# Performance work log

Measured on AMD Instinct MI355X. Metric: run time of the kernel, lower is better.

Reference implementation:

```python
import jax, jax.numpy as jnp
import numpy as np

B, L = 64, 2048
N_RESTYPE, N_GROUP, N_ATOM = 21, 8, 14


def _compose(R1, t1, R2, t2):
    # rigid compose: (R1,t1) o (R2,t2) = (R1@R2, R1@t2 + t1)
    R = jnp.einsum('...ij,...jk->...ik', R1, R2)
    t = jnp.einsum('...ij,...j->...i', R1, t2) + t1
    return R, t


def setup_inputs() -> dict:
    key = jax.random.key(0)
    ks = jax.random.split(key, 8)
    return {
        'bb_rots': jax.random.normal(ks[0], (B, L, 3, 3), jnp.float32),
        'bb_trans': jax.random.normal(ks[1], (B, L, 3), jnp.float32),
        'angles': jax.random.normal(ks[2], (B, L, 7, 2), jnp.float32),
        'aatype': jax.random.randint(ks[3], (B, L), 0, N_RESTYPE),
        'default_frames': jax.random.normal(ks[4], (N_RESTYPE, N_GROUP, 4, 4), jnp.float32),
        'group_idx': jax.random.randint(ks[5], (N_RESTYPE, N_ATOM), 0, N_GROUP),
        'atom_mask': jax.random.uniform(ks[6], (N_RESTYPE, N_ATOM), jnp.float32),
        'lit_positions': jax.random.normal(ks[7], (N_RESTYPE, N_ATOM, 3), jnp.float32),
    }


def reference(bb_rots, bb_trans, angles, aatype, default_frames, group_idx, atom_mask, lit_positions):
    # ---- torsion_angles_to_frames ----
    d4 = default_frames[aatype]                      # [B,L,8,4,4]
    dR, dt = d4[..., :3, :3], d4[..., :3, 3]
    # prepend identity backbone torsion (sin=0, cos=1)
    bb = jnp.broadcast_to(jnp.array([0.0, 1.0], angles.dtype), (*angles.shape[:-2], 1, 2))
    ang = jnp.concatenate([bb, angles], axis=-2)     # [B,L,8,2]
    s, c = ang[..., 0], ang[..., 1]
    z, o = jnp.zeros_like(s), jnp.ones_like(s)
    # rotation about x-axis built from (sin, cos)
    rotx = jnp.stack([
        jnp.stack([o, z, z], axis=-1),
        jnp.stack([z, c, -s], axis=-1),
        jnp.stack([z, s, c], axis=-1),
    ], axis=-2)                                      # [B,L,8,3,3]
    fR = jnp.einsum('blgij,blgjk->blgik', dR, rotx)  # default_r.compose(all_rots)
    ft = dt                                          # all_rots has zero translation
    # chain chi2..chi4 onto chi1
    R5, t5 = _compose(fR[:, :, 4], ft[:, :, 4], fR[:, :, 5], ft[:, :, 5])
    R6, t6 = _compose(R5, t5, fR[:, :, 6], ft[:, :, 6])
    R7, t7 = _compose(R6, t6, fR[:, :, 7], ft[:, :, 7])
    Rbb = jnp.concatenate([fR[:, :, :5], R5[:, :, None], R6[:, :, None], R7[:, :, None]], axis=2)
    tbb = jnp.concatenate([ft[:, :, :5], t5[:, :, None], t6[:, :, None], t7[:, :, None]], axis=2)
    # compose with global backbone frame
    Rg = jnp.einsum('blij,blgjk->blgik', bb_rots, Rbb)          # [B,L,8,3,3]
    tg = jnp.einsum('blij,blgj->blgi', bb_rots, tbb) + bb_trans[:, :, None]

    # ---- frames_and_literature_positions_to_atom14_pos ----
    gidx = group_idx[aatype]                                    # [B,L,14]
    Ra = jnp.take_along_axis(Rg, gidx[:, :, :, None, None], axis=2)  # [B,L,14,3,3]
    ta = jnp.take_along_axis(tg, gidx[:, :, :, None], axis=2)        # [B,L,14,3]
    lit = lit_positions[aatype]                                 # [B,L,14,3]
    mask = atom_mask[aatype][..., None]                         # [B,L,14,1]
    pred = jnp.einsum('blaij,blaj->blai', Ra, lit) + ta
    return pred * mask
```

## Files before the change

kernel.cpp:

```cpp
#include <hip/hip_runtime.h>


constexpr int NRES_TOTAL = 64 * 2048;
constexpr int NRT = 21;
constexpr int NG  = 8;
constexpr int NA  = 14;
constexpr int BLK = 256;
constexpr int RPB = BLK / 4;

__global__ __launch_bounds__(256) void protein_mapper_kernel(
    const float* __restrict__ bb_rots,
    const float* __restrict__ bb_trans,
    const float* __restrict__ angles,
    const int*   __restrict__ aatype,
    const float* __restrict__ default_frames,
    const int*   __restrict__ group_idx,
    const float* __restrict__ atom_mask,
    const float* __restrict__ lit_positions,
    float* __restrict__ out)
{
    __shared__ float s_frames[128 * NRT];
    __shared__ int   s_gidx[NA * NRT];
    __shared__ float s_mask[NA * NRT];
    __shared__ float s_lit[NA * 3 * NRT];

    const int t   = threadIdx.x;
    const int res = blockIdx.x * RPB + (t >> 2);
    const int sub = t & 3;

    const int aa_early = aatype[res];
    float2 ang[7];
    {
        const float2* angp = reinterpret_cast<const float2*>(angles + (size_t)res * 14);
        #pragma unroll
        for (int g = 0; g < 7; ++g) ang[g] = angp[g];
    }
    const float* br = bb_rots + (size_t)res * 9;
    const float b00 = br[0], b01 = br[1], b02 = br[2];
    const float b10 = br[3], b11 = br[4], b12 = br[5];
    const float b20 = br[6], b21 = br[7], b22 = br[8];
    const float* btp = bb_trans + (size_t)res * 3;
    const float bt0 = btp[0], bt1 = btp[1], bt2 = btp[2];

    for (int n = t; n < NRT * 128; n += BLK) {
        const int aa = n / 128, j = n % 128;
        s_frames[j * NRT + aa] = default_frames[n];
    }
    for (int n = t; n < NRT * NA; n += BLK) {
        const int aa = n / NA, a = n % NA;
        s_gidx[a * NRT + aa] = group_idx[n];
        s_mask[a * NRT + aa] = atom_mask[n];
    }
    for (int n = t; n < NRT * NA * 3; n += BLK) {
        const int aa = n / (NA * 3), k = n % (NA * 3);
        s_lit[k * NRT + aa] = lit_positions[n];
    }
    __syncthreads();

    const int aa = aa_early;

    float sv[NG], cv[NG];
    sv[0] = 0.0f; cv[0] = 1.0f;
    #pragma unroll
    for (int g = 1; g < NG; ++g) { sv[g] = ang[g - 1].x; cv[g] = ang[g - 1].y; }

    float G[NG][12];
    #pragma unroll
    for (int g = 0; g < NG; ++g) {
        const float cg = cv[g], sg = sv[g];
        #pragma unroll
        for (int r = 0; r < 3; ++r) {
            const float a0 = s_frames[(g * 16 + r * 4 + 0) * NRT + aa];
            const float a1 = s_frames[(g * 16 + r * 4 + 1) * NRT + aa];
            const float a2 = s_frames[(g * 16 + r * 4 + 2) * NRT + aa];
            const float a3 = s_frames[(g * 16 + r * 4 + 3) * NRT + aa];
            G[g][r * 3 + 0] = a0;
            G[g][r * 3 + 1] = cg * a1 + sg * a2;
            G[g][r * 3 + 2] = cg * a2 - sg * a1;
            G[g][9 + r]     = a3;
        }
    }

    #pragma unroll
    for (int g = 5; g < NG; ++g) {
        float Q[12];
        #pragma unroll
        for (int r = 0; r < 3; ++r) {
            const float p0 = G[g - 1][r * 3 + 0];
            const float p1 = G[g - 1][r * 3 + 1];
            const float p2 = G[g - 1][r * 3 + 2];
            #pragma unroll
            for (int cdx = 0; cdx < 3; ++cdx)
                Q[r * 3 + cdx] = p0 * G[g][cdx] + p1 * G[g][3 + cdx] + p2 * G[g][6 + cdx];
            Q[9 + r] = p0 * G[g][9] + p1 * G[g][10] + p2 * G[g][11] + G[g - 1][9 + r];
        }
        #pragma unroll
        for (int k = 0; k < 12; ++k) G[g][k] = Q[k];
    }

    float q[12];
    #pragma unroll
    for (int j = 0; j < 4; ++j) {
        const int a = 4 * sub + j;
        if (a < NA) {
            const int   ga = s_gidx[a * NRT + aa];
            const float m_ = s_mask[a * NRT + aa];
            const float lx = s_lit[(a * 3 + 0) * NRT + aa];
            const float ly = s_lit[(a * 3 + 1) * NRT + aa];
            const float lz = s_lit[(a * 3 + 2) * NRT + aa];
            const bool b0_ = ga & 1, b1_ = ga & 2, b2_ = ga & 4;
            float S[12];
            #pragma unroll
            for (int e = 0; e < 12; ++e) {
                const float t0 = b0_ ? G[1][e] : G[0][e];
                const float t1 = b0_ ? G[3][e] : G[2][e];
                const float t2 = b0_ ? G[5][e] : G[4][e];
                const float t3 = b0_ ? G[7][e] : G[6][e];
                const float u0 = b1_ ? t1 : t0;
                const float u1 = b1_ ? t3 : t2;
                S[e] = b2_ ? u1 : u0;
            }
            const float px = S[0] * lx + S[1] * ly + S[2] * lz + S[9];
            const float py = S[3] * lx + S[4] * ly + S[5] * lz + S[10];
            const float pz = S[6] * lx + S[7] * ly + S[8] * lz + S[11];
            q[j * 3 + 0] = (b00 * px + b01 * py + b02 * pz + bt0) * m_;
            q[j * 3 + 1] = (b10 * px + b11 * py + b12 * pz + bt1) * m_;
            q[j * 3 + 2] = (b20 * px + b21 * py + b22 * pz + bt2) * m_;
        }
    }

    float2* o2 = reinterpret_cast<float2*>(out) + (size_t)res * 21 + sub * 6;
    const int nf2 = (sub == 3) ? 3 : 6;
    #pragma unroll
    for (int k = 0; k < 6; ++k) {
        if (k < nf2) {
            float2 v; v.x = q[2 * k + 0]; v.y = q[2 * k + 1];
            o2[k] = v;
        }
    }
}

extern "C" void kernel_launch(void* const* d_in, const int* in_sizes, int n_in,
                              void* d_out, int out_size, void* d_ws, size_t ws_size,
                              hipStream_t stream) {
    const float* bb_rots        = (const float*)d_in[0];
    const float* bb_trans       = (const float*)d_in[1];
    const float* angles         = (const float*)d_in[2];
    const int*   aatype         = (const int*)d_in[3];
    const float* default_frames = (const float*)d_in[4];
    const int*   group_idx      = (const int*)d_in[5];
    const float* atom_mask      = (const float*)d_in[6];
    const float* lit_positions  = (const float*)d_in[7];
    float* out = (float*)d_out;

    const int blocks = NRES_TOTAL / RPB;
    protein_mapper_kernel<<<blocks, BLK, 0, stream>>>(
        bb_rots, bb_trans, angles, aatype,
        default_frames, group_idx, atom_mask, lit_positions, out);
}
```

Measured before the change: 106.5 us.

## Split per-residue frame work across eight threads with shared-memory frame exchange

Each residue is now handled by eight threads instead of four. Each thread builds one torsion group frame, the frames are exchanged through a new shared-memory buffer, and threads 5-7 compose the chi chain from it. Atoms are then assigned two per thread and look up their frame from shared memory instead of doing register select chains. This cuts per-thread register pressure and redundant frame computation, at the cost of extra __syncthreads, extra shared memory, uneven chain work, and scalar strided output stores in place of float2 stores.

```diff
diff --git a/kernel.cpp b/kernel.cpp
--- a/kernel.cpp
+++ b/kernel.cpp
@@ -5,10 +5,11 @@
 constexpr int NRT = 21;
 constexpr int NG  = 8;
 constexpr int NA  = 14;
-constexpr int BLK = 256;
-constexpr int RPB = BLK / 4;
+constexpr int BLK = 512;
+constexpr int RPB = BLK / NG;
+constexpr int RIG_STRIDE = 100;
 
-__global__ __launch_bounds__(256) void protein_mapper_kernel(
+__global__ __launch_bounds__(512) void protein_mapper_kernel(
     const float* __restrict__ bb_rots,
     const float* __restrict__ bb_trans,
     const float* __restrict__ angles,
@@ -23,25 +24,9 @@
     __shared__ int   s_gidx[NA * NRT];
     __shared__ float s_mask[NA * NRT];
     __shared__ float s_lit[NA * 3 * NRT];
+    __shared__ float s_rig[RPB * RIG_STRIDE];
 
-    const int t   = threadIdx.x;
-    const int res = blockIdx.x * RPB + (t >> 2);
-    const int sub = t & 3;
-
-    const int aa_early = aatype[res];
-    float2 ang[7];
-    {
-        const float2* angp = reinterpret_cast<const float2*>(angles + (size_t)res * 14);
-        #pragma unroll
-        for (int g = 0; g < 7; ++g) ang[g] = angp[g];
-    }
-    const float* br = bb_rots + (size_t)res * 9;
-    const float b00 = br[0], b01 = br[1], b02 = br[2];
-    const float b10 = br[3], b11 = br[4], b12 = br[5];
-    const float b20 = br[6], b21 = br[7], b22 = br[8];
-    const float* btp = bb_trans + (size_t)res * 3;
-    const float bt0 = btp[0], bt1 = btp[1], bt2 = btp[2];
-
+    const int t = threadIdx.x;
     for (int n = t; n < NRT * 128; n += BLK) {
         const int aa = n / 128, j = n % 128;
         s_frames[j * NRT + aa] = default_frames[n];
@@ -55,87 +40,103 @@
         const int aa = n / (NA * 3), k = n % (NA * 3);
         s_lit[k * NRT + aa] = lit_positions[n];
     }
+
+    const int lres = t >> 3;
+    const int sub  = t & 7;
+    const int res  = blockIdx.x * RPB + lres;
+    const int aa   = aatype[res];
+
+    float sg_ = 0.0f, cg_ = 1.0f;
+    if (sub != 0) {
+        const float2 sc = *reinterpret_cast<const float2*>(
+            angles + (size_t)res * 14 + (size_t)(sub - 1) * 2);
+        sg_ = sc.x; cg_ = sc.y;
+    }
     __syncthreads();
 
-    const int aa = aa_early;
+    float F[12];
+    #pragma unroll
+    for (int r = 0; r < 3; ++r) {
+        const float a0 = s_frames[(sub * 16 + r * 4 + 0) * NRT + aa];
+        const float a1 = s_frames[(sub * 16 + r * 4 + 1) * NRT + aa];
+        const float a2 = s_frames[(sub * 16 + r * 4 + 2) * NRT + aa];
+        const float a3 = s_frames[(sub * 16 + r * 4 + 3) * NRT + aa];
+        F[r * 3 + 0] = a0;
+        F[r * 3 + 1] = cg_ * a1 + sg_ * a2;
+        F[r * 3 + 2] = cg_ * a2 - sg_ * a1;
+        F[9 + r]     = a3;
+    }
 
-    float sv[NG], cv[NG];
-    sv[0] = 0.0f; cv[0] = 1.0f;
-    #pragma unroll
-    for (int g = 1; g < NG; ++g) { sv[g] = ang[g - 1].x; cv[g] = ang[g - 1].y; }
+    float* rig = s_rig + lres * RIG_STRIDE;
+    {
+        float4* dst = reinterpret_cast<float4*>(rig + sub * 12);
+        float4 w0; w0.x = F[0]; w0.y = F[1];  w0.z = F[2];  w0.w = F[3];
+        float4 w1; w1.x = F[4]; w1.y = F[5];  w1.z = F[6];  w1.w = F[7];
+        float4 w2; w2.x = F[8]; w2.y = F[9];  w2.z = F[10]; w2.w = F[11];
+        dst[0] = w0; dst[1] = w1; dst[2] = w2;
+    }
+    __syncthreads();
 
-    float G[NG][12];
-    #pragma unroll
-    for (int g = 0; g < NG; ++g) {
-        const float cg = cv[g], sg = sv[g];
-        #pragma unroll
-        for (int r = 0; r < 3; ++r) {
-            const float a0 = s_frames[(g * 16 + r * 4 + 0) * NRT + aa];
-            const float a1 = s_frames[(g * 16 + r * 4 + 1) * NRT + aa];
-            const float a2 = s_frames[(g * 16 + r * 4 + 2) * NRT + aa];
-            const float a3 = s_frames[(g * 16 + r * 4 + 3) * NRT + aa];
-            G[g][r * 3 + 0] = a0;
-            G[g][r * 3 + 1] = cg * a1 + sg * a2;
-            G[g][r * 3 + 2] = cg * a2 - sg * a1;
-            G[g][9 + r]     = a3;
+    float P[12];
+    if (sub >= 5) {
+        const float4* f4 = reinterpret_cast<const float4*>(rig + 4 * 12);
+        float4 p0 = f4[0], p1 = f4[1], p2 = f4[2];
+        P[0]=p0.x; P[1]=p0.y; P[2]=p0.z; P[3]=p0.w;
+        P[4]=p1.x; P[5]=p1.y; P[6]=p1.z; P[7]=p1.w;
+        P[8]=p2.x; P[9]=p2.y; P[10]=p2.z; P[11]=p2.w;
+        for (int g = 5; g <= sub; ++g) {
+            const float4* fg = reinterpret_cast<const float4*>(rig + g * 12);
+            const float4 l0 = fg[0], l1 = fg[1], l2 = fg[2];
+            const float L[12] = {l0.x,l0.y,l0.z,l0.w,l1.x,l1.y,l1.z,l1.w,
+                                 l2.x,l2.y,l2.z,l2.w};
+            float Q[12];
+            #pragma unroll
+            for (int r = 0; r < 3; ++r) {
+                const float p0_ = P[r*3+0], p1_ = P[r*3+1], p2_ = P[r*3+2];
+                #pragma unroll
+                for (int c = 0; c < 3; ++c)
+                    Q[r*3+c] = p0_ * L[c] + p1_ * L[3+c] + p2_ * L[6+c];
+                Q[9+r] = p0_ * L[9] + p1_ * L[10] + p2_ * L[11] + P[9+r];
+            }
+            #pragma unroll
+            for (int k = 0; k < 12; ++k) P[k] = Q[k];
         }
     }
+    __syncthreads();
+    if (sub >= 5) {
+        float4* dst = reinterpret_cast<float4*>(rig + sub * 12);
+        float4 w0; w0.x = P[0]; w0.y = P[1];  w0.z = P[2];  w0.w = P[3];
+        float4 w1; w1.x = P[4]; w1.y = P[5];  w1.z = P[6];  w1.w = P[7];
+        float4 w2; w2.x = P[8]; w2.y = P[9];  w2.z = P[10]; w2.w = P[11];
+        dst[0] = w0; dst[1] = w1; dst[2] = w2;
+    }
+    __syncthreads();
+
+    const float* br = bb_rots + (size_t)res * 9;
+    const float b00 = br[0], b01 = br[1], b02 = br[2];
+    const float b10 = br[3], b11 = br[4], b12 = br[5];
+    const float b20 = br[6], b21 = br[7], b22 = br[8];
+    const float* btp = bb_trans + (size_t)res * 3;
+    const float bt0 = btp[0], bt1 = btp[1], bt2 = btp[2];
 
     #pragma unroll
-    for (int g = 5; g < NG; ++g) {
-        float Q[12];
-        #pragma unroll
-        for (int r = 0; r < 3; ++r) {
-            const float p0 = G[g - 1][r * 3 + 0];
-            const float p1 = G[g - 1][r * 3 + 1];
-            const float p2 = G[g - 1][r * 3 + 2];
-            #pragma unroll
-            for (int cdx = 0; cdx < 3; ++cdx)
-                Q[r * 3 + cdx] = p0 * G[g][cdx] + p1 * G[g][3 + cdx] + p2 * G[g][6 + cdx];
-            Q[9 + r] = p0 * G[g][9] + p1 * G[g][10] + p2 * G[g][11] + G[g - 1][9 + r];
-        }
-        #pragma unroll
-        for (int k = 0; k < 12; ++k) G[g][k] = Q[k];
-    }
-
-    float q[12];
-    #pragma unroll
-    for (int j = 0; j < 4; ++j) {
-        const int a = 4 * sub + j;
+    for (int k = 0; k < 2; ++k) {
+        const int a = sub + k * 8;
         if (a < NA) {
             const int   ga = s_gidx[a * NRT + aa];
             const float m_ = s_mask[a * NRT + aa];
             const float lx = s_lit[(a * 3 + 0) * NRT + aa];
             const float ly = s_lit[(a * 3 + 1) * NRT + aa];
             const float lz = s_lit[(a * 3 + 2) * NRT + aa];
-            const bool b0_ = ga & 1, b1_ = ga & 2, b2_ = ga & 4;
-            float S[12];
-            #pragma unroll
-            for (int e = 0; e < 12; ++e) {
-                const float t0 = b0_ ? G[1][e] : G[0][e];
-                const float t1 = b0_ ? G[3][e] : G[2][e];
-                const float t2 = b0_ ? G[5][e] : G[4][e];
-                const float t3 = b0_ ? G[7][e] : G[6][e];
-                const float u0 = b1_ ? t1 : t0;
-                const float u1 = b1_ ? t3 : t2;
-                S[e] = b2_ ? u1 : u0;
-            }
-            const float px = S[0] * lx + S[1] * ly + S[2] * lz + S[9];
-            const float py = S[3] * lx + S[4] * ly + S[5] * lz + S[10];
-            const float pz = S[6] * lx + S[7] * ly + S[8] * lz + S[11];
-            q[j * 3 + 0] = (b00 * px + b01 * py + b02 * pz + bt0) * m_;
-            q[j * 3 + 1] = (b10 * px + b11 * py + b12 * pz + bt1) * m_;
-            q[j * 3 + 2] = (b20 * px + b21 * py + b22 * pz + bt2) * m_;
-        }
-    }
-
-    float2* o2 = reinterpret_cast<float2*>(out) + (size_t)res * 21 + sub * 6;
-    const int nf2 = (sub == 3) ? 3 : 6;
-    #pragma unroll
-    for (int k = 0; k < 6; ++k) {
-        if (k < nf2) {
-            float2 v; v.x = q[2 * k + 0]; v.y = q[2 * k + 1];
-            o2[k] = v;
+            const float4* fp = reinterpret_cast<const float4*>(rig + ga * 12);
+            const float4 f0 = fp[0], f1 = fp[1], f2 = fp[2];
+            const float px = f0.x * lx + f0.y * ly + f0.z * lz + f2.y;
+            const float py = f0.w * lx + f1.x * ly + f1.y * lz + f2.z;
+            const float pz = f1.z * lx + f1.w * ly + f2.x * lz + f2.w;
+            float* op = out + (size_t)res * (NA * 3) + a * 3;
+            op[0] = (b00 * px + b01 * py + b02 * pz + bt0) * m_;
+            op[1] = (b10 * px + b11 * py + b12 * pz + bt1) * m_;
+            op[2] = (b20 * px + b21 * py + b22 * pz + bt2) * m_;
         }
     }
 }
```

Result: faster. 100.7 us (-5.4%).
